# Kernel optimization log

Hardware: AMD Instinct MI355X
Metric: run time of the kernel (lower is better)

The kernel has to match this reference:

```python
import jax, jax.numpy as jnp
import numpy as np

B, S, H = 2, 2048, 1024
HFF = 4096
E, K = 8, 2

def setup_inputs() -> dict:
    key = jax.random.key(0)
    k1, k2, k3, k4, k5 = jax.random.split(key, 5)
    x = jax.random.normal(k1, (B, S, H), dtype=jnp.float32)
    topk_probs = jax.random.uniform(k2, (B, S, K), dtype=jnp.float32)
    topk_indices = jax.random.randint(k3, (B, S, K), 0, E, dtype=jnp.int64)
    stdv = 1.0 / np.sqrt(H)
    W1 = jax.random.uniform(k4, (E, HFF, H), minval=-stdv, maxval=stdv, dtype=jnp.float32)
    stdv2 = 1.0 / np.sqrt(HFF)
    W2 = jax.random.uniform(k5, (E, H, HFF), minval=-stdv2, maxval=stdv2, dtype=jnp.float32)
    return {"x": x, "topk_probs": topk_probs, "topk_indices": topk_indices, "W1": W1, "W2": W2}

def reference(x, topk_probs, topk_indices, W1, W2):
    # gate[b,s,e] = max_k topk_probs[b,s,k] * (topk_indices[b,s,k]==e)
    # (max over k, matching probs_mask.max(dim=-1) in the torch module)
    e_ids = jnp.arange(E, dtype=topk_indices.dtype)  # [E]
    sel = topk_indices[..., None] == e_ids  # [B,S,K,E]
    gate = jnp.max(jnp.where(sel, topk_probs[..., None], 0.0), axis=2)  # [B,S,E]
    # dense per-expert FFN over all tokens (as the original computes)
    h = jnp.einsum('bsh,efh->ebsf', x, W1)       # [E,B,S,HFF]
    h = jax.nn.gelu(h)
    y = jnp.einsum('ebsf,ehf->ebsh', h, W2)      # [E,B,S,H]
    # probability applied after FFN, masked combine over experts
    out = jnp.einsum('bse,ebsh->bsh', gate, y)   # [B,S,H]
    return out
```

## Files before the change

### kernel.cpp

```cpp
#include <hip/hip_runtime.h>

typedef unsigned short ushort_t;
typedef __attribute__((ext_vector_type(8))) short short8;
typedef __attribute__((ext_vector_type(4))) float f32x4;

#define TOKENS  4096
#define H_DIM   1024
#define HFF_DIM 4096
#define NEXP    8

__device__ __forceinline__ ushort_t f2b(float f) {
    union { float f; unsigned u; } v; v.f = f;
    unsigned r = v.u + 0x7fffu + ((v.u >> 16) & 1u);
    return (ushort_t)(r >> 16);
}

__device__ __forceinline__ float gelu_tanh(float x) {
    float u = 0.7978845608028654f * (x + 0.044715f * x * x * x);
    return 0.5f * x * (1.0f + tanhf(u));
}

__device__ __forceinline__ void gload16(const ushort_t* g, ushort_t* l) {
    __builtin_amdgcn_global_load_lds(
        (const __attribute__((address_space(1))) unsigned int*)g,
        (__attribute__((address_space(3))) unsigned int*)l,
        16, 0, 0);
}

__global__ void route_cvt_kernel(const float* __restrict__ probs,
                                 const int* __restrict__ idx,
                                 const float* __restrict__ x,
                                 ushort_t* __restrict__ xb,
                                 int* __restrict__ count,
                                 int* __restrict__ token_id,
                                 float* __restrict__ gate) {
    const int gid = blockIdx.x * blockDim.x + threadIdx.x;

    {
        const float4* s = (const float4*)(x + (size_t)gid * 8);
        float4 a = s[0], b = s[1];
        ushort_t o[8];
        o[0] = f2b(a.x); o[1] = f2b(a.y); o[2] = f2b(a.z); o[3] = f2b(a.w);
        o[4] = f2b(b.x); o[5] = f2b(b.y); o[6] = f2b(b.z); o[7] = f2b(b.w);
        *(short8*)(xb + (size_t)gid * 8) = *(short8*)o;
    }

    if (blockIdx.x >= TOKENS / 256) return;
    const int t = gid;
    const int lane = threadIdx.x & 63;

    const int i0 = idx[t * 2 + 0];
    const int i1 = idx[t * 2 + 1];
    const float p0 = probs[t * 2 + 0];
    const float p1 = probs[t * 2 + 1];
    const bool dup = (i0 == i1);
    const float q0 = dup ? fmaxf(p0, p1) : p0;

#pragma unroll
    for (int k = 0; k < 2; ++k) {
        const int want = (k == 0) ? i0 : (dup ? -1 : i1);
        const float p  = (k == 0) ? q0 : p1;
#pragma unroll
        for (int e = 0; e < NEXP; ++e) {
            unsigned long long m = __ballot(want == e);
            if (m == 0ull) continue;
            if (want == e) {
                const int lead = __ffsll((long long)m) - 1;
                int base = 0;
                if (lane == lead) base = atomicAdd(&count[e], (int)__popcll(m));
                base = __shfl(base, lead);
                const int pos = base + (int)__popcll(m & ((1ull << lane) - 1ull));
                token_id[e * TOKENS + pos] = t;
                gate[e * TOKENS + pos] = p;
            }
        }
    }
}

__global__ void cvt_kernel(const float* __restrict__ src, ushort_t* __restrict__ dst, int n8) {
    int i = blockIdx.x * blockDim.x + threadIdx.x;
    if (i >= n8) return;
    const float4* s = (const float4*)(src + (size_t)i * 8);
    float4 a = s[0], b = s[1];
    ushort_t o[8];
    o[0] = f2b(a.x); o[1] = f2b(a.y); o[2] = f2b(a.z); o[3] = f2b(a.w);
    o[4] = f2b(b.x); o[5] = f2b(b.y); o[6] = f2b(b.z); o[7] = f2b(b.w);
    *(short8*)(dst + (size_t)i * 8) = *(short8*)o;
}

__global__ __launch_bounds__(256) void gemm1_kernel(
        const ushort_t* __restrict__ xb, const ushort_t* __restrict__ W1b,
        const int* __restrict__ count, const int* __restrict__ token_id,
        ushort_t* __restrict__ h) {
    const int wg  = blockIdx.x;
    const int swz = (wg & 7) * (NEXP * 32 * 32 / 8) + (wg >> 3);
    const int e   = swz >> 10;
    const int rem = swz & 1023;
    const int mt  = rem >> 5;
    const int nt  = rem & 31;

    const int cnt = count[e];
    if (mt * 128 >= cnt) return;
    int base = 0;
    for (int i = 0; i < e; ++i) base += count[i];

    __shared__ __align__(16) ushort_t As[128 * 32];
    __shared__ __align__(16) ushort_t Bs[128 * 32];

    const int tid = threadIdx.x;
    const int lane = tid & 63;
    const int wave = tid >> 6;

    const int sr0 = (wave << 5) + (lane >> 2);
    const int sr1 = sr0 + 16;
    const int sc  = (lane & 3) << 3;

    int ra0 = mt * 128 + sr0; if (ra0 >= cnt) ra0 = cnt - 1;
    int ra1 = mt * 128 + sr1; if (ra1 >= cnt) ra1 = cnt - 1;
    const int t0 = token_id[e * TOKENS + ra0];
    const int t1 = token_id[e * TOKENS + ra1];
    const ushort_t* pa0 = xb + (size_t)t0 * H_DIM + sc;
    const ushort_t* pa1 = xb + (size_t)t1 * H_DIM + sc;
    const ushort_t* pb0 = W1b + (size_t)e * HFF_DIM * H_DIM
                          + (size_t)(nt * 128 + sr0) * H_DIM + sc;
    const ushort_t* pb1 = pb0 + (size_t)16 * H_DIM;
    ushort_t* lA0 = &As[wave << 10];
    ushort_t* lA1 = lA0 + 512;
    ushort_t* lB0 = &Bs[wave << 10];
    ushort_t* lB1 = lB0 + 512;

    const int wm = (wave >> 1) << 6;
    const int wn = (wave & 1) << 6;
    const int lr = lane & 15;
    const int lq = lane >> 4;

    f32x4 acc[4][4];
#pragma unroll
    for (int mi = 0; mi < 4; ++mi)
#pragma unroll
        for (int ni = 0; ni < 4; ++ni)
            acc[mi][ni] = (f32x4){0.f, 0.f, 0.f, 0.f};

    for (int k0 = 0; k0 < H_DIM; k0 += 32) {
        __syncthreads();
        gload16(pa0 + k0, lA0);
        gload16(pa1 + k0, lA1);
        gload16(pb0 + k0, lB0);
        gload16(pb1 + k0, lB1);
        __syncthreads();

        short8 af[4], bf[4];
#pragma unroll
        for (int mi = 0; mi < 4; ++mi)
            af[mi] = *(const short8*)&As[(wm + mi * 16 + lr) * 32 + lq * 8];
#pragma unroll
        for (int ni = 0; ni < 4; ++ni)
            bf[ni] = *(const short8*)&Bs[(wn + ni * 16 + lr) * 32 + lq * 8];
#pragma unroll
        for (int mi = 0; mi < 4; ++mi)
#pragma unroll
            for (int ni = 0; ni < 4; ++ni)
                acc[mi][ni] = __builtin_amdgcn_mfma_f32_16x16x32_bf16(
                    af[mi], bf[ni], acc[mi][ni], 0, 0, 0);
    }

#pragma unroll
    for (int mi = 0; mi < 4; ++mi) {
#pragma unroll
        for (int r = 0; r < 4; ++r) {
            int m = mt * 128 + wm + mi * 16 + lq * 4 + r;
            if (m < cnt) {
                ushort_t* hp = h + (size_t)(base + m) * HFF_DIM + nt * 128 + wn + lr;
#pragma unroll
                for (int ni = 0; ni < 4; ++ni)
                    hp[ni * 16] = f2b(gelu_tanh(acc[mi][ni][r]));
            }
        }
    }
}

__global__ __launch_bounds__(256) void gemm2_kernel(
        const ushort_t* __restrict__ h, const ushort_t* __restrict__ W2b,
        const int* __restrict__ count, const int* __restrict__ token_id,
        const float* __restrict__ gate, float* __restrict__ out) {
    const int wg  = blockIdx.x;
    const int swz = (wg & 7) * (NEXP * 32 * 8 / 8) + (wg >> 3);
    const int e   = swz >> 8;
    const int rem = swz & 255;
    const int mt  = rem >> 3;
    const int nt  = rem & 7;

    const int cnt = count[e];
    if (mt * 128 >= cnt) return;
    int base = 0;
    for (int i = 0; i < e; ++i) base += count[i];

    __shared__ __align__(16) ushort_t As[128 * 32];
    __shared__ __align__(16) ushort_t Bs[128 * 32];

    const int tid = threadIdx.x;
    const int lane = tid & 63;
    const int wave = tid >> 6;

    const int sr0 = (wave << 5) + (lane >> 2);
    const int sr1 = sr0 + 16;
    const int sc  = (lane & 3) << 3;

    int ra0 = mt * 128 + sr0; if (ra0 >= cnt) ra0 = cnt - 1;
    int ra1 = mt * 128 + sr1; if (ra1 >= cnt) ra1 = cnt - 1;
    const ushort_t* pa0 = h + (size_t)(base + ra0) * HFF_DIM + sc;
    const ushort_t* pa1 = h + (size_t)(base + ra1) * HFF_DIM + sc;
    const ushort_t* pb0 = W2b + (size_t)e * H_DIM * HFF_DIM
                          + (size_t)(nt * 128 + sr0) * HFF_DIM + sc;
    const ushort_t* pb1 = pb0 + (size_t)16 * HFF_DIM;
    ushort_t* lA0 = &As[wave << 10];
    ushort_t* lA1 = lA0 + 512;
    ushort_t* lB0 = &Bs[wave << 10];
    ushort_t* lB1 = lB0 + 512;

    const int wm = (wave >> 1) << 6;
    const int wn = (wave & 1) << 6;
    const int lr = lane & 15;
    const int lq = lane >> 4;

    f32x4 acc[4][4];
#pragma unroll
    for (int mi = 0; mi < 4; ++mi)
#pragma unroll
        for (int ni = 0; ni < 4; ++ni)
            acc[mi][ni] = (f32x4){0.f, 0.f, 0.f, 0.f};

    for (int k0 = 0; k0 < HFF_DIM; k0 += 32) {
        __syncthreads();
        gload16(pa0 + k0, lA0);
        gload16(pa1 + k0, lA1);
        gload16(pb0 + k0, lB0);
        gload16(pb1 + k0, lB1);
        __syncthreads();

        short8 af[4], bf[4];
#pragma unroll
        for (int mi = 0; mi < 4; ++mi)
            af[mi] = *(const short8*)&As[(wm + mi * 16 + lr) * 32 + lq * 8];
#pragma unroll
        for (int ni = 0; ni < 4; ++ni)
            bf[ni] = *(const short8*)&Bs[(wn + ni * 16 + lr) * 32 + lq * 8];
#pragma unroll
        for (int mi = 0; mi < 4; ++mi)
#pragma unroll
            for (int ni = 0; ni < 4; ++ni)
                acc[mi][ni] = __builtin_amdgcn_mfma_f32_16x16x32_bf16(
                    af[mi], bf[ni], acc[mi][ni], 0, 0, 0);
    }

#pragma unroll
    for (int mi = 0; mi < 4; ++mi) {
#pragma unroll
        for (int r = 0; r < 4; ++r) {
            int m = mt * 128 + wm + mi * 16 + lq * 4 + r;
            if (m < cnt) {
                int tok = token_id[e * TOKENS + m];
                float g = gate[e * TOKENS + m];
                float* op = out + (size_t)tok * H_DIM + nt * 128 + wn + lr;
#pragma unroll
                for (int ni = 0; ni < 4; ++ni)
                    atomicAdd(&op[ni * 16], g * acc[mi][ni][r]);
            }
        }
    }
}

extern "C" void kernel_launch(void* const* d_in, const int* in_sizes, int n_in,
                              void* d_out, int out_size, void* d_ws, size_t ws_size,
                              hipStream_t stream) {
    const float* x     = (const float*)d_in[0];
    const float* probs = (const float*)d_in[1];
    const int*   idx   = (const int*)d_in[2];
    const float* W1    = (const float*)d_in[3];
    const float* W2    = (const float*)d_in[4];
    float* out = (float*)d_out;

    char* ws = (char*)d_ws;
    int*      count    = (int*)ws;
    int*      token_id = (int*)(ws + 4096);
    float*    gate     = (float*)(ws + 4096 + 8 * TOKENS * 4);
    ushort_t* xb       = (ushort_t*)(ws + ((size_t)1 << 20));
    ushort_t* Wb       = (ushort_t*)(ws + ((size_t)1 << 20) + ((size_t)8 << 20));
    ushort_t* h        = (ushort_t*)(ws + ((size_t)1 << 20) + ((size_t)72 << 20));

    hipMemsetAsync(count, 0, 64, stream);
    hipMemsetAsync(out, 0, (size_t)out_size * sizeof(float), stream);

    route_cvt_kernel<<<TOKENS * H_DIM / 8 / 256, 256, 0, stream>>>(
        probs, idx, x, xb, count, token_id, gate);

    {
        int n8 = NEXP * HFF_DIM * H_DIM / 8;
        cvt_kernel<<<(n8 + 255) / 256, 256, 0, stream>>>(W1, Wb, n8);
    }

    gemm1_kernel<<<NEXP * 32 * 32, 256, 0, stream>>>(xb, Wb, count, token_id, h);

    {
        int n8 = NEXP * H_DIM * HFF_DIM / 8;
        cvt_kernel<<<(n8 + 255) / 256, 256, 0, stream>>>(W2, Wb, n8);
    }

    gemm2_kernel<<<NEXP * 32 * 8, 256, 0, stream>>>(h, Wb, count, token_id, gate, out);
}
```

Measured before the change: 536.8 us.

## Fuse W1 conversion into prep kernel and overlap W2 conversion with GEMM1

```diff
diff --git a/kernel.cpp b/kernel.cpp
--- a/kernel.cpp
+++ b/kernel.cpp
@@ -9,10 +9,26 @@
 #define HFF_DIM 4096
 #define NEXP    8
 
+#define XCVT_BLOCKS  (TOKENS * H_DIM / 8 / 256)
+#define W1CVT_BLOCKS (NEXP * HFF_DIM * H_DIM / 8 / 256)
+#define W2CVT_BLOCKS (NEXP * H_DIM * HFF_DIM / 8 / 256)
+#define G1_BLOCKS    (NEXP * 32 * 32)
+#define G2_BLOCKS    (NEXP * 32 * 8)
+
 __device__ __forceinline__ ushort_t f2b(float f) {
     union { float f; unsigned u; } v; v.f = f;
     unsigned r = v.u + 0x7fffu + ((v.u >> 16) & 1u);
     return (ushort_t)(r >> 16);
+}
+
+__device__ __forceinline__ void cvt8(const float* __restrict__ src,
+                                     ushort_t* __restrict__ dst, size_t i) {
+    const float4* s = (const float4*)(src + i * 8);
+    float4 a = s[0], b = s[1];
+    ushort_t o[8];
+    o[0] = f2b(a.x); o[1] = f2b(a.y); o[2] = f2b(a.z); o[3] = f2b(a.w);
+    o[4] = f2b(b.x); o[5] = f2b(b.y); o[6] = f2b(b.z); o[7] = f2b(b.w);
+    *(short8*)(dst + i * 8) = *(short8*)o;
 }
 
 __device__ __forceinline__ float gelu_tanh(float x) {
@@ -27,25 +43,24 @@
         16, 0, 0);
 }
 
-__global__ void route_cvt_kernel(const float* __restrict__ probs,
-                                 const int* __restrict__ idx,
-                                 const float* __restrict__ x,
-                                 ushort_t* __restrict__ xb,
-                                 int* __restrict__ count,
-                                 int* __restrict__ token_id,
-                                 float* __restrict__ gate) {
-    const int gid = blockIdx.x * blockDim.x + threadIdx.x;
-
-    {
-        const float4* s = (const float4*)(x + (size_t)gid * 8);
-        float4 a = s[0], b = s[1];
-        ushort_t o[8];
-        o[0] = f2b(a.x); o[1] = f2b(a.y); o[2] = f2b(a.z); o[3] = f2b(a.w);
-        o[4] = f2b(b.x); o[5] = f2b(b.y); o[6] = f2b(b.z); o[7] = f2b(b.w);
-        *(short8*)(xb + (size_t)gid * 8) = *(short8*)o;
-    }
-
-    if (blockIdx.x >= TOKENS / 256) return;
+__global__ void prep_kernel(const float* __restrict__ probs,
+                            const int* __restrict__ idx,
+                            const float* __restrict__ x,
+                            ushort_t* __restrict__ xb,
+                            const float* __restrict__ W1,
+                            ushort_t* __restrict__ W1b,
+                            int* __restrict__ count,
+                            int* __restrict__ token_id,
+                            float* __restrict__ gate) {
+    const int wg = blockIdx.x;
+    if (wg >= XCVT_BLOCKS) {
+        cvt8(W1, W1b, (size_t)(wg - XCVT_BLOCKS) * 256 + threadIdx.x);
+        return;
+    }
+    const int gid = wg * 256 + threadIdx.x;
+    cvt8(x, xb, (size_t)gid);
+
+    if (wg >= TOKENS / 256) return;
     const int t = gid;
     const int lane = threadIdx.x & 63;
 
@@ -80,20 +95,20 @@
 __global__ void cvt_kernel(const float* __restrict__ src, ushort_t* __restrict__ dst, int n8) {
     int i = blockIdx.x * blockDim.x + threadIdx.x;
     if (i >= n8) return;
-    const float4* s = (const float4*)(src + (size_t)i * 8);
-    float4 a = s[0], b = s[1];
-    ushort_t o[8];
-    o[0] = f2b(a.x); o[1] = f2b(a.y); o[2] = f2b(a.z); o[3] = f2b(a.w);
-    o[4] = f2b(b.x); o[5] = f2b(b.y); o[6] = f2b(b.z); o[7] = f2b(b.w);
-    *(short8*)(dst + (size_t)i * 8) = *(short8*)o;
+    cvt8(src, dst, (size_t)i);
 }
 
 __global__ __launch_bounds__(256) void gemm1_kernel(
         const ushort_t* __restrict__ xb, const ushort_t* __restrict__ W1b,
         const int* __restrict__ count, const int* __restrict__ token_id,
-        ushort_t* __restrict__ h) {
+        ushort_t* __restrict__ h,
+        const float* __restrict__ W2, ushort_t* __restrict__ W2b) {
+    if (blockIdx.x >= G1_BLOCKS) {
+        cvt8(W2, W2b, (size_t)(blockIdx.x - G1_BLOCKS) * 256 + threadIdx.x);
+        return;
+    }
     const int wg  = blockIdx.x;
-    const int swz = (wg & 7) * (NEXP * 32 * 32 / 8) + (wg >> 3);
+    const int swz = (wg & 7) * (G1_BLOCKS / 8) + (wg >> 3);
     const int e   = swz >> 10;
     const int rem = swz & 1023;
     const int mt  = rem >> 5;
@@ -184,7 +199,7 @@
         const int* __restrict__ count, const int* __restrict__ token_id,
         const float* __restrict__ gate, float* __restrict__ out) {
     const int wg  = blockIdx.x;
-    const int swz = (wg & 7) * (NEXP * 32 * 8 / 8) + (wg >> 3);
+    const int swz = (wg & 7) * (G2_BLOCKS / 8) + (wg >> 3);
     const int e   = swz >> 8;
     const int rem = swz & 255;
     const int mt  = rem >> 3;
@@ -285,26 +300,28 @@
     int*      token_id = (int*)(ws + 4096);
     float*    gate     = (float*)(ws + 4096 + 8 * TOKENS * 4);
     ushort_t* xb       = (ushort_t*)(ws + ((size_t)1 << 20));
-    ushort_t* Wb       = (ushort_t*)(ws + ((size_t)1 << 20) + ((size_t)8 << 20));
-    ushort_t* h        = (ushort_t*)(ws + ((size_t)1 << 20) + ((size_t)72 << 20));
+    ushort_t* W1b      = (ushort_t*)(ws + ((size_t)9 << 20));
+
+    const bool overlap = ws_size >= ((size_t)201 << 20);
+    ushort_t* W2b = overlap ? (ushort_t*)(ws + ((size_t)73 << 20)) : W1b;
+    ushort_t* h   = overlap ? (ushort_t*)(ws + ((size_t)137 << 20))
+                            : (ushort_t*)(ws + ((size_t)73 << 20));
 
     hipMemsetAsync(count, 0, 64, stream);
     hipMemsetAsync(out, 0, (size_t)out_size * sizeof(float), stream);
 
-    route_cvt_kernel<<<TOKENS * H_DIM / 8 / 256, 256, 0, stream>>>(
-        probs, idx, x, xb, count, token_id, gate);
-
-    {
-        int n8 = NEXP * HFF_DIM * H_DIM / 8;
-        cvt_kernel<<<(n8 + 255) / 256, 256, 0, stream>>>(W1, Wb, n8);
-    }
-
-    gemm1_kernel<<<NEXP * 32 * 32, 256, 0, stream>>>(xb, Wb, count, token_id, h);
-
-    {
+    prep_kernel<<<XCVT_BLOCKS + W1CVT_BLOCKS, 256, 0, stream>>>(
+        probs, idx, x, xb, W1, W1b, count, token_id, gate);
+
+    if (overlap) {
+        gemm1_kernel<<<G1_BLOCKS + W2CVT_BLOCKS, 256, 0, stream>>>(
+            xb, W1b, count, token_id, h, W2, W2b);
+    } else {
+        gemm1_kernel<<<G1_BLOCKS, 256, 0, stream>>>(
+            xb, W1b, count, token_id, h, W2, W2b);
         int n8 = NEXP * H_DIM * HFF_DIM / 8;
-        cvt_kernel<<<(n8 + 255) / 256, 256, 0, stream>>>(W2, Wb, n8);
-    }
-
-    gemm2_kernel<<<NEXP * 32 * 8, 256, 0, stream>>>(h, Wb, count, token_id, gate, out);
-}
+        cvt_kernel<<<(n8 + 255) / 256, 256, 0, stream>>>(W2, W2b, n8);
+    }
+
+    gemm2_kernel<<<G2_BLOCKS, 256, 0, stream>>>(h, W2b, count, token_id, gate, out);
+}
```

Result: no change. 535.2 us (-0.3%).
